# Kernel optimization log

Measured on AMD Instinct MI355X. Metric: run time of the kernel, lower is better.

Reference implementation:

```python
import jax, jax.numpy as jnp
import numpy as np

NUM_PITCHES = 128
RHYTHM_DIM = 10
HARMONY_DIM = 12
VOCAB_SIZE = 390
EPS = 1e-08


def setup_inputs() -> dict:
    key = jax.random.key(0)
    k_tok, k_w1, k_w2 = jax.random.split(key, 3)
    B, T = 1024, 8192
    stats_dim = NUM_PITCHES + RHYTHM_DIM + HARMONY_DIM  # 150
    midi_tokens = jax.random.randint(k_tok, (B, T), 0, VOCAB_SIZE, dtype=jnp.int64 if jax.config.jax_enable_x64 else jnp.int32)
    W1 = jax.random.normal(k_w1, (stats_dim, 256), dtype=jnp.float32) * 0.05
    b1 = jnp.zeros((256,), dtype=jnp.float32)
    W2 = jax.random.normal(k_w2, (256, 128), dtype=jnp.float32) * 0.05
    b2 = jnp.zeros((128,), dtype=jnp.float32)
    return {"midi_tokens": midi_tokens, "W1": W1, "b1": b1, "W2": W2, "b2": b2}


def _compute_stats(midi_tokens):
    """Vectorized pitch histogram + rhythm + harmony stats. midi_tokens: (B, T) int."""
    B, T = midi_tokens.shape
    # Pitch distribution: histogram of tokens % 128 per batch row, via one flat scatter-add.
    pitch = midi_tokens % NUM_PITCHES  # (B, T) in [0, 128)
    flat_bins = (jnp.arange(B, dtype=pitch.dtype)[:, None] * NUM_PITCHES + pitch).reshape(-1)
    hist = jnp.zeros((B * NUM_PITCHES,), dtype=jnp.float32).at[flat_bins].add(1.0)
    pitch_dist = hist.reshape(B, NUM_PITCHES)
    pitch_dist = pitch_dist / (pitch_dist.sum(axis=-1, keepdims=True) + EPS)
    # Rhythm: mean and (unbiased, torch-default) std; remaining 8 dims are zeros.
    tf = midi_tokens.astype(jnp.float32)
    mean = tf.mean(axis=-1)
    std = jnp.sqrt(((tf - mean[:, None]) ** 2).sum(axis=-1) / (T - 1))
    rhythm = jnp.zeros((B, RHYTHM_DIM), dtype=jnp.float32)
    rhythm = rhythm.at[:, 0].set(mean).at[:, 1].set(std)
    # Harmony: original uses torch.rand(12) per row; deterministic uniform here.
    harmony = jax.random.uniform(jax.random.key(42), (B, HARMONY_DIM), dtype=jnp.float32)
    return jnp.concatenate([pitch_dist, rhythm, harmony], axis=-1)  # (B, 150)


def reference(midi_tokens, W1, b1, W2, b2):
    stats = _compute_stats(midi_tokens)
    h = jax.nn.relu(stats @ W1 + b1)
    return h @ W2 + b2  # (B, feature_dim=128)
```

## Files before the change

### kernel.cpp

```cpp
#include <hip/hip_runtime.h>
#include <stdint.h>
#include <math.h>

#define T_SEQ 8192

typedef int vint4 __attribute__((ext_vector_type(4)));

__device__ __forceinline__ uint32_t rotl32(uint32_t x, int n) {
    return (x << n) | (x >> (32 - n));
}

__device__ uint32_t jax_threefry_bits_12288(uint32_t idx) {
    const uint32_t k0 = 0u, k1 = 42u, k2 = 0u ^ 42u ^ 0x1BD11BDAu;
    uint32_t i = (idx < 6144u) ? idx : (idx - 6144u);
    uint32_t x0 = i + k0;
    uint32_t x1 = (i + 6144u) + k1;
#define TF_R4(a,b,c,d) \
    x0 += x1; x1 = rotl32(x1, a); x1 ^= x0; \
    x0 += x1; x1 = rotl32(x1, b); x1 ^= x0; \
    x0 += x1; x1 = rotl32(x1, c); x1 ^= x0; \
    x0 += x1; x1 = rotl32(x1, d); x1 ^= x0;
    TF_R4(13, 15, 26, 6);   x0 += k1; x1 += k2 + 1u;
    TF_R4(17, 29, 16, 24);  x0 += k2; x1 += k0 + 2u;
    TF_R4(13, 15, 26, 6);   x0 += k0; x1 += k1 + 3u;
    TF_R4(17, 29, 16, 24);  x0 += k1; x1 += k2 + 4u;
    TF_R4(13, 15, 26, 6);   x0 += k2; x1 += k0 + 5u;
#undef TF_R4
    return (idx < 6144u) ? x0 : x1;
}

__global__ __launch_bounds__(512) void fused_kernel(const int* __restrict__ tok,
                                                    const float* __restrict__ W1,
                                                    const float* __restrict__ b1,
                                                    const float* __restrict__ W2,
                                                    const float* __restrict__ b2,
                                                    float* __restrict__ out) {
    const int tid = threadIdx.x;
    const int wave = tid >> 6;
    const int r0 = blockIdx.x * 2;

    __shared__ int hist[8][128];
    __shared__ int wsum[8];
    __shared__ unsigned wsq[8];
    __shared__ float s[2][150];
    __shared__ float h[2][256];
    __shared__ float part[2][128];

    for (int i = tid; i < 1024; i += 512) ((int*)hist)[i] = 0;
    __syncthreads();

    {
        const int row_local = tid >> 8;
        const int t256 = tid & 255;
        const vint4* tp = (const vint4*)(tok + (size_t)(r0 + row_local) * T_SEQ);
        int sum = 0;
        unsigned sq = 0;
#pragma unroll
        for (int j = 0; j < 8; ++j) {
            vint4 v = __builtin_nontemporal_load(&tp[j * 256 + t256]);
            atomicAdd(&hist[wave][v.x & 127], 1); sum += v.x; sq += (unsigned)__mul24(v.x, v.x);
            atomicAdd(&hist[wave][v.y & 127], 1); sum += v.y; sq += (unsigned)__mul24(v.y, v.y);
            atomicAdd(&hist[wave][v.z & 127], 1); sum += v.z; sq += (unsigned)__mul24(v.z, v.z);
            atomicAdd(&hist[wave][v.w & 127], 1); sum += v.w; sq += (unsigned)__mul24(v.w, v.w);
        }
#pragma unroll
        for (int off = 32; off > 0; off >>= 1) {
            sum += __shfl_down(sum, off);
            sq  += __shfl_down(sq, off);
        }
        if ((tid & 63) == 0) { wsum[wave] = sum; wsq[wave] = sq; }
    }
    __syncthreads();

    if (tid < 300) {
        const int r = tid >= 150;
        const int k = tid - r * 150;
        const int wb = r * 4;
        float val;
        if (k < 128) {
            int hh = hist[wb][k] + hist[wb + 1][k] + hist[wb + 2][k] + hist[wb + 3][k];
            val = (float)hh * (1.0f / 8192.0f);
        } else if (k == 128) {
            int ss = wsum[wb] + wsum[wb + 1] + wsum[wb + 2] + wsum[wb + 3];
            val = (float)ss * (1.0f / 8192.0f);
        } else if (k == 129) {
            double ss = (double)(wsum[wb] + wsum[wb + 1] + wsum[wb + 2] + wsum[wb + 3]);
            double qq = (double)wsq[wb] + (double)wsq[wb + 1] + (double)wsq[wb + 2] + (double)wsq[wb + 3];
            val = (float)sqrt((qq - ss * ss / 8192.0) / 8191.0);
        } else if (k < 138) {
            val = 0.0f;
        } else {
            uint32_t bits = jax_threefry_bits_12288((uint32_t)(r0 + r) * 12u + (uint32_t)(k - 138));
            val = __uint_as_float((bits >> 9) | 0x3f800000u) - 1.0f;
        }
        s[r][k] = val;
    }
    __syncthreads();

    {
        const int g = tid >> 8, c = tid & 255;
        float acc = b1[c];
#pragma unroll 5
        for (int k = 0; k < 150; ++k)
            acc = fmaf(s[g][k], W1[k * 256 + c], acc);
        h[g][c] = fmaxf(acc, 0.0f);
    }
    __syncthreads();

    {
        const int half = tid >> 8, g = (tid >> 7) & 1, c = tid & 127;
        const float* hr = h[g];
        const int kb = half * 128;
        float acc = half ? 0.0f : b2[c];
#pragma unroll 8
        for (int k = 0; k < 128; ++k)
            acc = fmaf(hr[kb + k], W2[(kb + k) * 128 + c], acc);
        if (half) part[g][c] = acc;
        __syncthreads();
        if (!half) out[(r0 + g) * 128 + c] = acc + part[g][c];
    }
}

extern "C" void kernel_launch(void* const* d_in, const int* in_sizes, int n_in,
                              void* d_out, int out_size, void* d_ws, size_t ws_size,
                              hipStream_t stream) {
    const int*   tok = (const int*)d_in[0];
    const float* W1  = (const float*)d_in[1];
    const float* b1  = (const float*)d_in[2];
    const float* W2  = (const float*)d_in[3];
    const float* b2  = (const float*)d_in[4];
    float* out = (float*)d_out;

    fused_kernel<<<512, 512, 0, stream>>>(tok, W1, b1, W2, b2, out);
}
```

Baseline: 98.36 us.

## Process four rows per block to reuse weight loads across rows

Each block now handles four batch rows instead of two, and the grid shrinks to 256 blocks. In the first MLP layer each thread computes two rows and shares each W1 load between them. The second layer drops its split-K partial-sum stage and the extra barrier, with one thread per output computing the full 256-long dot product. This halves the total weight traffic, but there are now fewer blocks than the 256 CUs can absorb, so latency hiding on the 32 MB token stream drops and the serial MLP tail per block gets longer.

```diff
diff --git a/kernel.cpp b/kernel.cpp
--- a/kernel.cpp
+++ b/kernel.cpp
@@ -37,27 +37,26 @@
                                                     float* __restrict__ out) {
     const int tid = threadIdx.x;
     const int wave = tid >> 6;
-    const int r0 = blockIdx.x * 2;
+    const int r0 = blockIdx.x * 4;
 
     __shared__ int hist[8][128];
     __shared__ int wsum[8];
     __shared__ unsigned wsq[8];
-    __shared__ float s[2][150];
-    __shared__ float h[2][256];
-    __shared__ float part[2][128];
+    __shared__ float s[4][150];
+    __shared__ float h[4][256];
 
     for (int i = tid; i < 1024; i += 512) ((int*)hist)[i] = 0;
     __syncthreads();
 
     {
-        const int row_local = tid >> 8;
-        const int t256 = tid & 255;
+        const int row_local = tid >> 7;
+        const int t128 = tid & 127;
         const vint4* tp = (const vint4*)(tok + (size_t)(r0 + row_local) * T_SEQ);
         int sum = 0;
         unsigned sq = 0;
 #pragma unroll
-        for (int j = 0; j < 8; ++j) {
-            vint4 v = __builtin_nontemporal_load(&tp[j * 256 + t256]);
+        for (int j = 0; j < 16; ++j) {
+            vint4 v = __builtin_nontemporal_load(&tp[j * 128 + t128]);
             atomicAdd(&hist[wave][v.x & 127], 1); sum += v.x; sq += (unsigned)__mul24(v.x, v.x);
             atomicAdd(&hist[wave][v.y & 127], 1); sum += v.y; sq += (unsigned)__mul24(v.y, v.y);
             atomicAdd(&hist[wave][v.z & 127], 1); sum += v.z; sq += (unsigned)__mul24(v.z, v.z);
@@ -72,20 +71,20 @@
     }
     __syncthreads();
 
-    if (tid < 300) {
-        const int r = tid >= 150;
-        const int k = tid - r * 150;
-        const int wb = r * 4;
+    for (int i = tid; i < 600; i += 512) {
+        const int r = i / 150;
+        const int k = i - r * 150;
+        const int wb = r * 2;
         float val;
         if (k < 128) {
-            int hh = hist[wb][k] + hist[wb + 1][k] + hist[wb + 2][k] + hist[wb + 3][k];
+            int hh = hist[wb][k] + hist[wb + 1][k];
             val = (float)hh * (1.0f / 8192.0f);
         } else if (k == 128) {
-            int ss = wsum[wb] + wsum[wb + 1] + wsum[wb + 2] + wsum[wb + 3];
+            int ss = wsum[wb] + wsum[wb + 1];
             val = (float)ss * (1.0f / 8192.0f);
         } else if (k == 129) {
-            double ss = (double)(wsum[wb] + wsum[wb + 1] + wsum[wb + 2] + wsum[wb + 3]);
-            double qq = (double)wsq[wb] + (double)wsq[wb + 1] + (double)wsq[wb + 2] + (double)wsq[wb + 3];
+            double ss = (double)(wsum[wb] + wsum[wb + 1]);
+            double qq = (double)wsq[wb] + (double)wsq[wb + 1];
             val = (float)sqrt((qq - ss * ss / 8192.0) / 8191.0);
         } else if (k < 138) {
             val = 0.0f;
@@ -99,25 +98,26 @@
 
     {
         const int g = tid >> 8, c = tid & 255;
-        float acc = b1[c];
+        float a0 = b1[c], a1 = a0;
 #pragma unroll 5
-        for (int k = 0; k < 150; ++k)
-            acc = fmaf(s[g][k], W1[k * 256 + c], acc);
-        h[g][c] = fmaxf(acc, 0.0f);
+        for (int k = 0; k < 150; ++k) {
+            float w = W1[k * 256 + c];
+            a0 = fmaf(s[2 * g][k], w, a0);
+            a1 = fmaf(s[2 * g + 1][k], w, a1);
+        }
+        h[2 * g][c] = fmaxf(a0, 0.0f);
+        h[2 * g + 1][c] = fmaxf(a1, 0.0f);
     }
     __syncthreads();
 
     {
-        const int half = tid >> 8, g = (tid >> 7) & 1, c = tid & 127;
-        const float* hr = h[g];
-        const int kb = half * 128;
-        float acc = half ? 0.0f : b2[c];
+        const int r = tid >> 7, c = tid & 127;
+        const float* hr = h[r];
+        float acc = b2[c];
 #pragma unroll 8
-        for (int k = 0; k < 128; ++k)
-            acc = fmaf(hr[kb + k], W2[(kb + k) * 128 + c], acc);
-        if (half) part[g][c] = acc;
-        __syncthreads();
-        if (!half) out[(r0 + g) * 128 + c] = acc + part[g][c];
+        for (int k = 0; k < 256; ++k)
+            acc = fmaf(hr[k], W2[k * 128 + c], acc);
+        out[(r0 + r) * 128 + c] = acc;
     }
 }
 
@@ -131,5 +131,5 @@
     const float* b2  = (const float*)d_in[4];
     float* out = (float*)d_out;
 
-    fused_kernel<<<512, 512, 0, stream>>>(tok, W1, b1, W2, b2, out);
+    fused_kernel<<<256, 512, 0, stream>>>(tok, W1, b1, W2, b2, out);
 }
```

Result: slower. 104.5 us (+6.3%).
